# Kernel optimization log

Hardware: AMD Instinct MI355X
Metric: run time of the kernel (lower is better)

The kernel has to match this reference:

```python
import jax, jax.numpy as jnp
import numpy as np

HIDDEN = 512
HEADS = 8
HEAD_DIM = HIDDEN // HEADS
MAX_DIST = 10
B, N = 16, 512
EPS = 1e-5


def _layer_norm(x, g, b):
    mu = jnp.mean(x, axis=-1, keepdims=True)
    var = jnp.mean(jnp.square(x - mu), axis=-1, keepdims=True)
    return (x - mu) * jax.lax.rsqrt(var + EPS) * g + b


def setup_inputs() -> dict:
    key = jax.random.key(0)
    ks = jax.random.split(key, 16)
    s = 0.02
    inp = {
        "x": jax.random.normal(ks[0], (B, N, HIDDEN), jnp.float32),
        "distances": jax.random.randint(ks[1], (B, N, N), 0, MAX_DIST, jnp.int32),
        "edge_features": jax.random.normal(ks[2], (B, N, N), jnp.float32),
        "attn_mask": jax.random.randint(ks[3], (B, N), 0, 2).astype(bool),
        "Wq": jax.random.normal(ks[4], (HIDDEN, HIDDEN), jnp.float32) * s,
        "bq": jnp.zeros((HIDDEN,), jnp.float32),
        "Wk": jax.random.normal(ks[5], (HIDDEN, HIDDEN), jnp.float32) * s,
        "bk": jnp.zeros((HIDDEN,), jnp.float32),
        "Wv": jax.random.normal(ks[6], (HIDDEN, HIDDEN), jnp.float32) * s,
        "bv": jnp.zeros((HIDDEN,), jnp.float32),
        "Wo": jax.random.normal(ks[7], (HIDDEN, HIDDEN), jnp.float32) * s,
        "bo": jnp.zeros((HIDDEN,), jnp.float32),
        "spatial_emb": jax.random.normal(ks[8], (MAX_DIST, HEADS), jnp.float32) * s,
        "edge_w": jax.random.normal(ks[9], (HEADS,), jnp.float32) * s,
        "edge_b": jnp.zeros((HEADS,), jnp.float32),
        "ln1_g": jnp.ones((HIDDEN,), jnp.float32),
        "ln1_b": jnp.zeros((HIDDEN,), jnp.float32),
        "ln2_g": jnp.ones((HIDDEN,), jnp.float32),
        "ln2_b": jnp.zeros((HIDDEN,), jnp.float32),
        "W1": jax.random.normal(ks[10], (HIDDEN, 4 * HIDDEN), jnp.float32) * s,
        "b1": jnp.zeros((4 * HIDDEN,), jnp.float32),
        "W2": jax.random.normal(ks[11], (4 * HIDDEN, HIDDEN), jnp.float32) * s,
        "b2": jnp.zeros((HIDDEN,), jnp.float32),
    }
    return inp


def reference(x, distances, edge_features, attn_mask, Wq, bq, Wk, bk, Wv, bv,
              Wo, bo, spatial_emb, edge_w, edge_b, ln1_g, ln1_b, ln2_g, ln2_b,
              W1, b1, W2, b2):
    b, n, _ = x.shape
    q = (x @ Wq + bq).reshape(b, n, HEADS, HEAD_DIM)
    k = (x @ Wk + bk).reshape(b, n, HEADS, HEAD_DIM)
    v = (x @ Wv + bv).reshape(b, n, HEADS, HEAD_DIM)
    # [b, h, i, j] attention scores
    scores = jnp.einsum('bihd,bjhd->bhij', q, k) / np.sqrt(HEAD_DIM).astype(np.float32)
    spatial_bias = spatial_emb[distances]                       # [b, i, j, h]
    edge_bias = edge_features[..., None] * edge_w + edge_b      # [b, i, j, h]
    scores = scores + jnp.transpose(spatial_bias + edge_bias, (0, 3, 1, 2))
    scores = jnp.where(attn_mask[:, None, None, :], -jnp.inf, scores)
    attn = jax.nn.softmax(scores, axis=-1)
    out = jnp.einsum('bhij,bjhd->bihd', attn, v).reshape(b, n, HIDDEN)
    out = out @ Wo + bo
    h = _layer_norm(x + out, ln1_g, ln1_b)
    ffn = jax.nn.relu(h @ W1 + b1) @ W2 + b2
    return _layer_norm(h + ffn, ln2_g, ln2_b)
```

## Files before the change

### kernel.cpp

```cpp
#include <hip/hip_runtime.h>
#include <stdint.h>
#include <stddef.h>

#define SEQ   512
#define HID   512
#define NHEAD 8
#define HD    64
#define NBATCH 16
#define NTOK  8192
#define MAXD  10

typedef __attribute__((ext_vector_type(8))) short short8;
typedef __attribute__((ext_vector_type(4))) float f32x4;

typedef __attribute__((address_space(3))) void        as3_void;
typedef const __attribute__((address_space(1))) void  as1_cvoid;

#define MFMA16(a,b,c) __builtin_amdgcn_mfma_f32_16x16x32_bf16((a),(b),(c),0,0,0)

__device__ __forceinline__ float bf2f(uint16_t u){ return __uint_as_float(((uint32_t)u)<<16); }
__device__ __forceinline__ uint16_t f2bf(float f){
  uint32_t i = __float_as_uint(f);
  return (uint16_t)((i + 0x7fffu + ((i>>16)&1u)) >> 16);
}

enum { EPI_BF16=0, EPI_F32=3, EPI_RELU=4 };

__global__ __launch_bounds__(256) void f2bf_kernel(
    const float* __restrict__ in, uint16_t* __restrict__ out, int n4)
{
  int i = blockIdx.x*256 + threadIdx.x;
  if (i < n4){
    float4 v = *(const float4*)(in + (size_t)i*4);
    *(ushort4*)(out + (size_t)i*4) =
        make_ushort4(f2bf(v.x), f2bf(v.y), f2bf(v.z), f2bf(v.w));
  }
}

__global__ __launch_bounds__(256) void transpose_all(
    const float* __restrict__ Wq, const float* __restrict__ Wk,
    const float* __restrict__ Wv, const float* __restrict__ Wo,
    const float* __restrict__ W1, const float* __restrict__ W2,
    uint16_t* __restrict__ tq, uint16_t* __restrict__ tk,
    uint16_t* __restrict__ tv, uint16_t* __restrict__ to_,
    uint16_t* __restrict__ t1, uint16_t* __restrict__ t2)
{
  __shared__ uint16_t tile[32][33];
  int id = blockIdx.x;
  const float* in; uint16_t* out; int R, C, tx, ty;
  if (id < 1024) {
    int m = id >> 8, loc = id & 255;
    in  = (m==0)?Wq:(m==1)?Wk:(m==2)?Wv:Wo;
    out = (m==0)?tq:(m==1)?tk:(m==2)?tv:to_;
    R = 512; C = 512; ty = loc>>4; tx = loc&15;
  } else if (id < 2048) {
    int loc = id-1024; in=W1; out=t1; R=512; C=2048; ty=loc>>6; tx=loc&63;
  } else {
    int loc = id-2048; in=W2; out=t2; R=2048; C=512; ty=loc>>4; tx=loc&15;
  }
  int bx = tx*32, by = ty*32;
  int lx = threadIdx.x & 31, ly = threadIdx.x >> 5;
  #pragma unroll
  for (int i=ly; i<32; i+=8) tile[i][lx] = f2bf(in[(size_t)(by+i)*C + bx+lx]);
  __syncthreads();
  #pragma unroll
  for (int i=ly; i<32; i+=8) out[(size_t)(bx+i)*R + by+lx] = tile[lx][i];
}

__global__ __launch_bounds__(512) void pack_bias(
    const int*   __restrict__ dist,
    const float* __restrict__ edge,
    const int*   __restrict__ mask,
    uint32_t*    __restrict__ outp)
{
  __shared__ int   dl[16][260];
  __shared__ float el[16][260];
  __shared__ int   ml[512];
  const int b  = blockIdx.y;
  const int it = blockIdx.x;
  const int t  = threadIdx.x;
  ml[t] = mask[b*SEQ + t];

  #pragma unroll
  for (int jh=0; jh<2; ++jh){
    if (jh) __syncthreads();
    {
      const int r  = t >> 5;
      const int c0 = (t & 31) * 8;
      const size_t g = ((size_t)b*SEQ + it*16 + r)*SEQ + jh*256 + c0;
      *(int4*)&dl[r][c0]     = *(const int4*)&dist[g];
      *(int4*)&dl[r][c0+4]   = *(const int4*)&dist[g+4];
      *(float4*)&el[r][c0]   = *(const float4*)&edge[g];
      *(float4*)&el[r][c0+4] = *(const float4*)&edge[g+4];
    }
    __syncthreads();
    {
      const int i   = t & 15;
      const int j0p = (t >> 4) * 8;
      const int jt  = jh*4 + (j0p >> 6);
      const int jn  = (j0p >> 4) & 3;
      const int lg  = (j0p & 15) >> 2;
      uint32_t w[8];
      #pragma unroll
      for (int e=0; e<8; ++e){
        const int jl = j0p + e;
        const int jg = jh*256 + jl;
        const uint32_t d  = (uint32_t)dl[i][jl] & 0xFFu;
        const uint32_t mk = (ml[jg] ? 1u : 0u) << 8;
        w[e] = ((uint32_t)f2bf(el[i][jl]) << 16) | mk | d;
      }
      uint32_t* ob = outp + ((((size_t)b*32 + it)*8 + jt)*64)*16;
      const int lane0 = lg*16 + i, lane1 = (lg+1)*16 + i;
      *(uint4*)&ob[lane0*16 + jn*4] = make_uint4(w[0],w[1],w[2],w[3]);
      *(uint4*)&ob[lane1*16 + jn*4] = make_uint4(w[4],w[5],w[6],w[7]);
    }
  }
}

template<int BM, int BN>
__device__ __forceinline__ void gemm_tile_mainloop(
    const uint16_t* __restrict__ A, const uint16_t* __restrict__ Bt,
    int K, int m0, int n0, uint16_t* lA, uint16_t* lB,
    f32x4 acc[4][(BM==128)?4:((BN==128)?2:1)])
{
  constexpr int NJ  = (BM==128)?4:((BN==128)?2:1);
  constexpr int ARD = BM/32;
  constexpr int BRD = BN/32;
  const int t = threadIdx.x;
  const int w = t>>6, l = t&63;
  const int lg = l>>4, lc = l&15;
  const int wr = (BM==128)?(w>>1):0;
  const int wc = (BM==128)?(w&1):w;
  const int swz = lc & 7;
  const int kSteps = K>>6;
  for (int kt=0; kt<kSteps; ++kt){
    const int k0 = kt<<6;
    #pragma unroll
    for (int rd=0; rd<ARD; ++rd){
      const int e   = rd*2048 + t*8;
      const int row = e>>6;
      const int col = (((e>>3)&7) ^ (row&7))*8;
      const uint16_t* ga = A + (size_t)(m0+row)*K + (k0+col);
      char* la = (char*)lA + rd*4096 + w*1024;
      __builtin_amdgcn_global_load_lds((as1_cvoid*)ga, (as3_void*)la, 16, 0, 0);
    }
    #pragma unroll
    for (int rd=0; rd<BRD; ++rd){
      const int e   = rd*2048 + t*8;
      const int row = e>>6;
      const int col = (((e>>3)&7) ^ (row&7))*8;
      const uint16_t* gb = Bt + (size_t)(n0+row)*K + (k0+col);
      char* lb = (char*)lB + rd*4096 + w*1024;
      __builtin_amdgcn_global_load_lds((as1_cvoid*)gb, (as3_void*)lb, 16, 0, 0);
    }
    __syncthreads();
    #pragma unroll
    for (int kk=0; kk<2; ++kk){
      const int cc = (kk*4 + lg) ^ swz;
      short8 af[4], bfr[NJ];
      #pragma unroll
      for (int i=0;i<4;i++)
        af[i]  = *(const short8*)&lA[(wr*64 + i*16 + lc)*64 + cc*8];
      #pragma unroll
      for (int j=0;j<NJ;j++)
        bfr[j] = *(const short8*)&lB[(wc*16*NJ + j*16 + lc)*64 + cc*8];
      #pragma unroll
      for (int i=0;i<4;i++)
        #pragma unroll
        for (int j=0;j<NJ;j++)
          acc[i][j] = MFMA16(af[i], bfr[j], acc[i][j]);
    }
    __syncthreads();
  }
}

template<int EPI, int BM, int BN>
__global__ __launch_bounds__(256,2) void gemm_bt(
    const uint16_t* __restrict__ A, const uint16_t* __restrict__ Bt,
    const float* __restrict__ bias, void* __restrict__ outp,
    int M, int N, int K)
{
  constexpr int NJ = (BM==128)?4:((BN==128)?2:1);
  __shared__ uint16_t lA[BM*64];
  __shared__ uint16_t lB[BN*64];
  f32x4 acc[4][NJ];
  #pragma unroll
  for (int i=0;i<4;i++)
    #pragma unroll
    for (int j=0;j<NJ;j++){ f32x4 z = {0.f,0.f,0.f,0.f}; acc[i][j]=z; }
  const int m0 = blockIdx.x*BM, n0 = blockIdx.y*BN;
  gemm_tile_mainloop<BM,BN>(A, Bt, K, m0, n0, lA, lB, acc);

  const int t=threadIdx.x, w=t>>6, l=t&63, lg=l>>4, lc=l&15;
  const int wr=(BM==128)?(w>>1):0, wc=(BM==128)?(w&1):w;
  #pragma unroll
  for (int j=0;j<NJ;j++){
    const int col = n0 + wc*16*NJ + j*16 + lc;
    const float bs = bias[col];
    #pragma unroll
    for (int i=0;i<4;i++){
      const int rowb = m0 + wr*64 + i*16 + lg*4;
      #pragma unroll
      for (int r=0;r<4;r++){
        float v = acc[i][j][r] + bs;
        if constexpr (EPI==EPI_RELU)   v = fmaxf(v, 0.f);
        if constexpr (EPI==EPI_F32)
          ((float*)outp)[(size_t)(rowb+r)*N + col] = v;
        else
          ((uint16_t*)outp)[(size_t)(rowb+r)*N + col] = f2bf(v);
      }
    }
  }
}

__global__ __launch_bounds__(256,2) void qkv_gemm(
    const uint16_t* __restrict__ x,
    const uint16_t* __restrict__ wtq, const uint16_t* __restrict__ wtk,
    const uint16_t* __restrict__ wtv,
    const float* __restrict__ bq, const float* __restrict__ bk,
    const float* __restrict__ bv,
    uint16_t* __restrict__ qo, uint16_t* __restrict__ kp,
    uint16_t* __restrict__ vp)
{
  __shared__ uint16_t lA[128*64];
  __shared__ uint16_t lB[128*64];
  const int z = blockIdx.z;
  const uint16_t* Bt = (z==0)?wtq:(z==1)?wtk:wtv;
  const float*  bias = (z==0)?bq :(z==1)?bk :bv;
  f32x4 acc[4][4];
  #pragma unroll
  for (int i=0;i<4;i++)
    #pragma unroll
    for (int j=0;j<4;j++){ f32x4 zz = {0.f,0.f,0.f,0.f}; acc[i][j]=zz; }
  const int m0 = blockIdx.x*128, n0 = blockIdx.y*128;
  gemm_tile_mainloop<128,128>(x, Bt, HID, m0, n0, lA, lB, acc);

  const int t=threadIdx.x, w=t>>6, l=t&63, lg=l>>4, lc=l&15, wr=w>>1, wc=w&1;
  if (z==0){
    const float scale = 0.125f;
    #pragma unroll
    for (int j=0;j<4;j++){
      const int col = n0 + wc*64 + j*16 + lc;
      const float bs = bias[col];
      #pragma unroll
      for (int i=0;i<4;i++){
        const int rowb = m0 + wr*64 + i*16 + lg*4;
        #pragma unroll
        for (int r=0;r<4;r++)
          qo[(size_t)(rowb+r)*HID + col] = f2bf((acc[i][j][r] + bs)*scale);
      }
    }
  } else if (z==1){
    #pragma unroll
    for (int j=0;j<4;j++){
      const int col = n0 + wc*64 + j*16 + lc;
      const float bs = bias[col];
      const int h_ = col>>6, cm = col&63, kk = cm>>5, lgk = (cm>>3)&3, e = col&7;
      #pragma unroll
      for (int i=0;i<4;i++){
        const int rowb = m0 + wr*64 + i*16 + lg*4;
        #pragma unroll
        for (int r=0;r<4;r++){
          const int tok = rowb + r;
          const int b_ = tok>>9, tl = tok&511;
          const int jt = tl>>6, jn = (tl>>4)&3, lck = tl&15;
          kp[((((size_t)(b_*8+h_)*8 + jt)*4 + jn)*2 + kk)*512
             + (lgk*16 + lck)*8 + e] = f2bf(acc[i][j][r] + bs);
        }
      }
    }
  } else {
    #pragma unroll
    for (int j=0;j<4;j++){
      const int col = n0 + wc*64 + j*16 + lc;
      const float bs = bias[col];
      const int h_ = col>>6, dn = (col>>4)&3, lcv = col&15;
      #pragma unroll
      for (int i=0;i<4;i++){
        const int rowb = m0 + wr*64 + i*16 + lg*4;
        const int b_ = rowb>>9, tl = rowb&511;
        const int jt = tl>>6, kk = (tl>>5)&1, lgv = (tl>>3)&3, e0 = tl&7;
        *(ushort4*)&vp[((((size_t)(b_*8+h_)*8 + jt)*2 + kk)*4 + dn)*512
                       + (lgv*16 + lcv)*8 + e0] =
            make_ushort4(f2bf(acc[i][j][0]+bs), f2bf(acc[i][j][1]+bs),
                         f2bf(acc[i][j][2]+bs), f2bf(acc[i][j][3]+bs));
      }
    }
  }
}

__global__ __launch_bounds__(512,4) void attn_kernel(
    const uint16_t* __restrict__ q,
    const uint16_t* __restrict__ kp,
    const uint16_t* __restrict__ vp,
    const uint32_t* __restrict__ biasp,
    const float*    __restrict__ semb,
    const float*    __restrict__ ew,
    const float*    __restrict__ eb,
    uint16_t* __restrict__ out)
{
  __shared__ float sp_rep[NHEAD][32][11];
  __shared__ uint16_t plds[NHEAD][2][16*64];
  const int b  = blockIdx.y;
  const int it = blockIdx.x;
  const int i0 = it*16;
  const int t  = threadIdx.x;
  const int h  = t>>6, l = t&63, lg = l>>4, lc = l&15;
  for (int i = t; i < NHEAD*32*MAXD; i += 512){
    const int hh = i / (32*MAXD), rem = i % (32*MAXD);
    const int a = rem / MAXD, d = rem % MAXD;
    sp_rep[hh][a][d] = semb[d*NHEAD + hh];
  }
  __syncthreads();
  const float ewf = ew[h], ebf = eb[h];
  const float* spl = &sp_rep[h][l&31][0];
  char* pbase = (char*)&plds[h][0][0];
  const int swz = (lc&7)<<4;

  short8 qf[2];
  #pragma unroll
  for (int kk=0;kk<2;kk++)
    qf[kk] = *(const short8*)&q[(size_t)(b*SEQ + i0 + lc)*HID + h*HD + kk*32 + lg*8];

  const uint4* bp = (const uint4*)(biasp + (((size_t)b*32 + it)*8)*64*16);
  const uint16_t* kpb = kp + (size_t)(b*8+h)*8*4*2*512 + l*8;
  const uint16_t* vpb = vp + (size_t)(b*8+h)*8*2*4*512 + l*8;

  float mrun[2] = {-1e30f, -1e30f};
  float lrun[2] = {0.f, 0.f};
  f32x4 oacc[2][4];
  #pragma unroll
  for (int s=0;s<2;s++)
    #pragma unroll
    for (int dn=0;dn<4;dn++){ f32x4 z={0.f,0.f,0.f,0.f}; oacc[s][dn]=z; }

  #pragma unroll
  for (int p=0; p<4; ++p){
    #pragma unroll
    for (int s=0; s<2; ++s){
      const int jt = s*4 + p;
      uint32_t uw[16];
      {
        const uint4* bq_ = bp + (jt*64 + l)*4;
        *(uint4*)&uw[0]  = bq_[0];
        *(uint4*)&uw[4]  = bq_[1];
        *(uint4*)&uw[8]  = bq_[2];
        *(uint4*)&uw[12] = bq_[3];
      }
      f32x4 st[4];
      #pragma unroll
      for (int jn=0;jn<4;jn++){ f32x4 z={0.f,0.f,0.f,0.f}; st[jn]=z; }
      __builtin_amdgcn_s_setprio(1);
      #pragma unroll
      for (int jn=0;jn<4;jn++){
        #pragma unroll
        for (int kk=0;kk<2;kk++){
          short8 kf = *(const short8*)&kpb[(size_t)((jt*4 + jn)*2 + kk)*512];
          st[jn] = MFMA16(kf, qf[kk], st[jn]);
        }
      }
      __builtin_amdgcn_s_setprio(0);
      float tmax = -1e30f;
      #pragma unroll
      for (int jn=0;jn<4;jn++){
        #pragma unroll
        for (int r=0;r<4;r++){
          const uint32_t u = uw[jn*4+r];
          float sv = st[jn][r] + spl[u & 0xFFu]
                   + bf2f((uint16_t)(u >> 16))*ewf + ebf;
          if (u & 0x100u) sv = -1e30f;
          st[jn][r] = sv;
          tmax = fmaxf(tmax, sv);
        }
      }
      {
        float tm = fmaxf(tmax, __shfl_xor(tmax, 16, 64));
        tm = fmaxf(tm, __shfl_xor(tm, 32, 64));
        float mnew = fmaxf(mrun[s], tm);
        mnew = fmaxf(mnew, -1e20f);
        const float c = __expf(mrun[s] - mnew);
        mrun[s] = mnew;
        float lsum = 0.f;
        char* pb = pbase + s*(16*64*2) + lc*128;
        #pragma unroll
        for (int jn=0;jn<4;jn++){
          float p0 = __expf(st[jn][0]-mnew);
          float p1 = __expf(st[jn][1]-mnew);
          float p2 = __expf(st[jn][2]-mnew);
          float p3 = __expf(st[jn][3]-mnew);
          lsum += (p0+p1)+(p2+p3);
          *(ushort4*)(pb + (((jn*16 + lg*4)*2) ^ swz)) =
              make_ushort4(f2bf(p0), f2bf(p1), f2bf(p2), f2bf(p3));
        }
        lrun[s] = lrun[s]*c + lsum;
        #pragma unroll
        for (int r=0;r<4;r++){
          const float cr = __shfl(c, lg*4+r, 64);
          #pragma unroll
          for (int dn=0;dn<4;dn++) oacc[s][dn][r] *= cr;
        }
      }
    }
    #pragma unroll
    for (int s=0; s<2; ++s){
      const int jt = s*4 + p;
      char* pb = pbase + s*(16*64*2) + lc*128;
      __builtin_amdgcn_s_setprio(1);
      #pragma unroll
      for (int kk=0;kk<2;kk++){
        short8 pa = *(const short8*)(pb + (((kk*32 + lg*8)*2) ^ swz));
        #pragma unroll
        for (int dn=0;dn<4;dn++){
          short8 vb = *(const short8*)&vpb[(size_t)((jt*2 + kk)*4 + dn)*512];
          oacc[s][dn] = MFMA16(pa, vb, oacc[s][dn]);
        }
      }
      __builtin_amdgcn_s_setprio(0);
    }
  }
  {
    const float mm = fmaxf(mrun[0], mrun[1]);
    const float c0 = __expf(mrun[0]-mm), c1 = __expf(mrun[1]-mm);
    float ls = lrun[0]*c0 + lrun[1]*c1;
    ls += __shfl_xor(ls, 16, 64);
    ls += __shfl_xor(ls, 32, 64);
    const float inv = 1.f/ls;
    #pragma unroll
    for (int r=0;r<4;r++){
      const float cr0 = __shfl(c0, lg*4+r, 64);
      const float cr1 = __shfl(c1, lg*4+r, 64);
      const float ir  = __shfl(inv, lg*4+r, 64);
      const size_t orow = ((size_t)b*SEQ + i0 + lg*4 + r)*HID;
      #pragma unroll
      for (int dn=0;dn<4;dn++)
        out[orow + h*HD + dn*16 + lc] =
            f2bf((oacc[0][dn][r]*cr0 + oacc[1][dn][r]*cr1)*ir);
    }
  }
}

__global__ __launch_bounds__(256) void ln_kernel(
    const float* __restrict__ a, const float* __restrict__ bsrc,
    const float* __restrict__ g, const float* __restrict__ bb,
    float* __restrict__ of, uint16_t* __restrict__ ob)
{
  const int row = blockIdx.x*4 + (threadIdx.x>>6);
  const int l = threadIdx.x & 63;
  const float* ar = a    + (size_t)row*HID;
  const float* br = bsrc + (size_t)row*HID;
  float u[8];
  {
    float4 a0 = *(const float4*)(ar + l*4);
    float4 a1 = *(const float4*)(ar + 256 + l*4);
    float4 b0 = *(const float4*)(br + l*4);
    float4 b1 = *(const float4*)(br + 256 + l*4);
    u[0]=a0.x+b0.x; u[1]=a0.y+b0.y; u[2]=a0.z+b0.z; u[3]=a0.w+b0.w;
    u[4]=a1.x+b1.x; u[5]=a1.y+b1.y; u[6]=a1.z+b1.z; u[7]=a1.w+b1.w;
  }
  float s=0.f, ss=0.f;
  #pragma unroll
  for (int e=0;e<8;e++){ s += u[e]; ss += u[e]*u[e]; }
  #pragma unroll
  for (int off=32; off>=1; off>>=1){
    s  += __shfl_xor(s,  off, 64);
    ss += __shfl_xor(ss, off, 64);
  }
  const float mu  = s*(1.f/512.f);
  const float inv = rsqrtf(ss*(1.f/512.f) - mu*mu + 1e-5f);
  float y[8];
  #pragma unroll
  for (int e=0;e<4;e++){
    int c0 = l*4+e, c1 = 256+l*4+e;
    y[e]   = (u[e]  -mu)*inv*g[c0] + bb[c0];
    y[4+e] = (u[4+e]-mu)*inv*g[c1] + bb[c1];
  }
  if (of){
    float* orow = of + (size_t)row*HID;
    *(float4*)(orow + l*4)       = make_float4(y[0],y[1],y[2],y[3]);
    *(float4*)(orow + 256 + l*4) = make_float4(y[4],y[5],y[6],y[7]);
  }
  if (ob){
    uint16_t* brow = ob + (size_t)row*HID;
    *(ushort4*)(brow + l*4)       = make_ushort4(f2bf(y[0]),f2bf(y[1]),f2bf(y[2]),f2bf(y[3]));
    *(ushort4*)(brow + 256 + l*4) = make_ushort4(f2bf(y[4]),f2bf(y[5]),f2bf(y[6]),f2bf(y[7]));
  }
}

extern "C" void kernel_launch(void* const* d_in, const int* in_sizes, int n_in,
                              void* d_out, int out_size, void* d_ws, size_t ws_size,
                              hipStream_t stream)
{
  (void)in_sizes; (void)n_in; (void)out_size; (void)ws_size;
  const float* x    = (const float*)d_in[0];
  const int*   dist = (const int*)  d_in[1];
  const float* edge = (const float*)d_in[2];
  const int*   mask = (const int*)  d_in[3];
  const float* Wq = (const float*)d_in[4];
  const float* bq = (const float*)d_in[5];
  const float* Wk = (const float*)d_in[6];
  const float* bk = (const float*)d_in[7];
  const float* Wv = (const float*)d_in[8];
  const float* bv = (const float*)d_in[9];
  const float* Wo = (const float*)d_in[10];
  const float* bo = (const float*)d_in[11];
  const float* semb = (const float*)d_in[12];
  const float* ew   = (const float*)d_in[13];
  const float* eb   = (const float*)d_in[14];
  const float* ln1g = (const float*)d_in[15];
  const float* ln1b = (const float*)d_in[16];
  const float* ln2g = (const float*)d_in[17];
  const float* ln2b = (const float*)d_in[18];
  const float* W1 = (const float*)d_in[19];
  const float* b1 = (const float*)d_in[20];
  const float* W2 = (const float*)d_in[21];
  const float* b2 = (const float*)d_in[22];

  char* ws = (char*)d_ws;
  uint16_t* xb16  = (uint16_t*)ws;
  uint16_t* qbuf  = xb16  + (size_t)NTOK*HID;
  uint16_t* kpbuf = qbuf  + (size_t)NTOK*HID;
  uint16_t* vpbuf = kpbuf + (size_t)NTOK*HID;
  uint16_t* aobuf = vpbuf + (size_t)NTOK*HID;
  uint16_t* f1buf = qbuf;
  uint32_t* biasp = (uint32_t*)(ws + (size_t)5*NTOK*HID*2);
  float*    tbuf  = (float*)biasp;
  float*    t2buf = tbuf;
  float*    hbuf  = tbuf + (size_t)NTOK*HID;
  uint16_t* hb16  = (uint16_t*)(hbuf + (size_t)NTOK*HID);
  uint16_t* wt    = hb16 + (size_t)NTOK*HID;
  uint16_t* wtq = wt;
  uint16_t* wtk = wtq + 512*512;
  uint16_t* wtv = wtk + 512*512;
  uint16_t* wto = wtv + 512*512;
  uint16_t* wt1 = wto + 512*512;
  uint16_t* wt2 = wt1 + 512*2048;

  pack_bias<<<dim3(32,16), 512, 0, stream>>>(dist, edge, mask, biasp);

  transpose_all<<<3072, 256, 0, stream>>>(Wq,Wk,Wv,Wo,W1,W2, wtq,wtk,wtv,wto,wt1,wt2);

  f2bf_kernel<<<4096, 256, 0, stream>>>(x, xb16, NTOK*HID/4);

  qkv_gemm<<<dim3(64,4,3), 256, 0, stream>>>(xb16, wtq,wtk,wtv, bq,bk,bv,
                                             qbuf, kpbuf, vpbuf);

  attn_kernel<<<dim3(32,16), 512, 0, stream>>>(qbuf, kpbuf, vpbuf, biasp,
                                               semb, ew, eb, aobuf);

  gemm_bt<EPI_F32,64,64><<<dim3(128,8), 256, 0, stream>>>(aobuf, wto, bo, tbuf, NTOK, HID, HID);

  ln_kernel<<<2048, 256, 0, stream>>>(tbuf, x, ln1g, ln1b, hbuf, hb16);

  gemm_bt<EPI_RELU,128,128><<<dim3(64,16), 256, 0, stream>>>(hb16, wt1, b1, f1buf, NTOK, 2048, HID);

  gemm_bt<EPI_F32,64,64><<<dim3(128,8), 256, 0, stream>>>(f1buf, wt2, b2, t2buf, NTOK, HID, 2048);

  ln_kernel<<<2048, 256, 0, stream>>>(t2buf, hbuf, ln2g, ln2b, (float*)d_out, nullptr);
}
```

Baseline: 163.2 us.

## Double-buffer GEMM LDS tiles and streamline attention softmax with exp2 and lazy rescale

The GEMM mainloop now double-buffers its LDS tiles, issuing the global-to-LDS loads for the next K step before computing on the current one, which doubles shared memory per block. The attention kernel folds log2(e) into the Q scale and the bias tables and uses exp2. It merges the edge bias into the spatial table, packs bf16 pairs with v_cvt_pk_bf16, and skips the running-max rescale when the tile max stays within a threshold of the current max. The lazy rescale lets probabilities exceed 1 by up to 2^8, which risks a small change in precision, and the larger LDS footprint may reduce occupancy.

Measured after the change: 194.0 us. +18.8%, slower.

```diff
diff --git a/kernel.cpp b/kernel.cpp
--- a/kernel.cpp
+++ b/kernel.cpp
@@ -9,6 +9,7 @@
 #define NBATCH 16
 #define NTOK  8192
 #define MAXD  10
+#define LOG2E 1.4426950408889634f
 
 typedef __attribute__((ext_vector_type(8))) short short8;
 typedef __attribute__((ext_vector_type(4))) float f32x4;
@@ -22,6 +23,11 @@
 __device__ __forceinline__ uint16_t f2bf(float f){
   uint32_t i = __float_as_uint(f);
   return (uint16_t)((i + 0x7fffu + ((i>>16)&1u)) >> 16);
+}
+__device__ __forceinline__ uint32_t cvt_pk_bf16(float lo, float hi){
+  uint32_t r;
+  asm("v_cvt_pk_bf16_f32 %0, %1, %2" : "=v"(r) : "v"(lo), "v"(hi));
+  return r;
 }
 
 enum { EPI_BF16=0, EPI_F32=3, EPI_RELU=4 };
@@ -133,7 +139,8 @@
   const int wc = (BM==128)?(w&1):w;
   const int swz = lc & 7;
   const int kSteps = K>>6;
-  for (int kt=0; kt<kSteps; ++kt){
+
+  auto stage = [&](int kt, int buf){
     const int k0 = kt<<6;
     #pragma unroll
     for (int rd=0; rd<ARD; ++rd){
@@ -141,7 +148,7 @@
       const int row = e>>6;
       const int col = (((e>>3)&7) ^ (row&7))*8;
       const uint16_t* ga = A + (size_t)(m0+row)*K + (k0+col);
-      char* la = (char*)lA + rd*4096 + w*1024;
+      char* la = (char*)(lA + buf*(BM*64)) + rd*4096 + w*1024;
       __builtin_amdgcn_global_load_lds((as1_cvoid*)ga, (as3_void*)la, 16, 0, 0);
     }
     #pragma unroll
@@ -150,20 +157,28 @@
       const int row = e>>6;
       const int col = (((e>>3)&7) ^ (row&7))*8;
       const uint16_t* gb = Bt + (size_t)(n0+row)*K + (k0+col);
-      char* lb = (char*)lB + rd*4096 + w*1024;
+      char* lb = (char*)(lB + buf*(BN*64)) + rd*4096 + w*1024;
       __builtin_amdgcn_global_load_lds((as1_cvoid*)gb, (as3_void*)lb, 16, 0, 0);
     }
-    __syncthreads();
+  };
+
+  stage(0, 0);
+  __syncthreads();
+  int cur = 0;
+  for (int kt=0; kt<kSteps; ++kt){
+    if (kt+1 < kSteps) stage(kt+1, cur^1);
+    const uint16_t* rA = lA + cur*(BM*64);
+    const uint16_t* rB = lB + cur*(BN*64);
     #pragma unroll
     for (int kk=0; kk<2; ++kk){
       const int cc = (kk*4 + lg) ^ swz;
       short8 af[4], bfr[NJ];
       #pragma unroll
       for (int i=0;i<4;i++)
-        af[i]  = *(const short8*)&lA[(wr*64 + i*16 + lc)*64 + cc*8];
+        af[i]  = *(const short8*)&rA[(wr*64 + i*16 + lc)*64 + cc*8];
       #pragma unroll
       for (int j=0;j<NJ;j++)
-        bfr[j] = *(const short8*)&lB[(wc*16*NJ + j*16 + lc)*64 + cc*8];
+        bfr[j] = *(const short8*)&rB[(wc*16*NJ + j*16 + lc)*64 + cc*8];
       #pragma unroll
       for (int i=0;i<4;i++)
         #pragma unroll
@@ -171,6 +186,7 @@
           acc[i][j] = MFMA16(af[i], bfr[j], acc[i][j]);
     }
     __syncthreads();
+    cur ^= 1;
   }
 }
 
@@ -181,8 +197,8 @@
     int M, int N, int K)
 {
   constexpr int NJ = (BM==128)?4:((BN==128)?2:1);
-  __shared__ uint16_t lA[BM*64];
-  __shared__ uint16_t lB[BN*64];
+  __shared__ uint16_t lA[2*BM*64];
+  __shared__ uint16_t lB[2*BN*64];
   f32x4 acc[4][NJ];
   #pragma unroll
   for (int i=0;i<4;i++)
@@ -222,8 +238,8 @@
     uint16_t* __restrict__ qo, uint16_t* __restrict__ kp,
     uint16_t* __restrict__ vp)
 {
-  __shared__ uint16_t lA[128*64];
-  __shared__ uint16_t lB[128*64];
+  __shared__ uint16_t lA[2*128*64];
+  __shared__ uint16_t lB[2*128*64];
   const int z = blockIdx.z;
   const uint16_t* Bt = (z==0)?wtq:(z==1)?wtk:wtv;
   const float*  bias = (z==0)?bq :(z==1)?bk :bv;
@@ -237,7 +253,7 @@
 
   const int t=threadIdx.x, w=t>>6, l=t&63, lg=l>>4, lc=l&15, wr=w>>1, wc=w&1;
   if (z==0){
-    const float scale = 0.125f;
+    const float scale = 0.125f * LOG2E;
     #pragma unroll
     for (int j=0;j<4;j++){
       const int col = n0 + wc*64 + j*16 + lc;
@@ -309,10 +325,10 @@
   for (int i = t; i < NHEAD*32*MAXD; i += 512){
     const int hh = i / (32*MAXD), rem = i % (32*MAXD);
     const int a = rem / MAXD, d = rem % MAXD;
-    sp_rep[hh][a][d] = semb[d*NHEAD + hh];
+    sp_rep[hh][a][d] = (semb[d*NHEAD + hh] + eb[hh]) * LOG2E;
   }
   __syncthreads();
-  const float ewf = ew[h], ebf = eb[h];
+  const float ewf = ew[h] * LOG2E;
   const float* spl = &sp_rep[h][l&31][0];
   char* pbase = (char*)&plds[h][0][0];
   const int swz = (lc&7)<<4;
@@ -367,7 +383,7 @@
         for (int r=0;r<4;r++){
           const uint32_t u = uw[jn*4+r];
           float sv = st[jn][r] + spl[u & 0xFFu]
-                   + bf2f((uint16_t)(u >> 16))*ewf + ebf;
+                   + bf2f((uint16_t)(u >> 16))*ewf;
           if (u & 0x100u) sv = -1e30f;
           st[jn][r] = sv;
           tmax = fmaxf(tmax, sv);
@@ -376,28 +392,34 @@
       {
         float tm = fmaxf(tmax, __shfl_xor(tmax, 16, 64));
         tm = fmaxf(tm, __shfl_xor(tm, 32, 64));
-        float mnew = fmaxf(mrun[s], tm);
-        mnew = fmaxf(mnew, -1e20f);
-        const float c = __expf(mrun[s] - mnew);
-        mrun[s] = mnew;
+        const bool need = !__all((tm <= mrun[s] + 8.0f) && (mrun[s] > -1e25f));
+        float c = 1.f;
+        if (need){
+          float mnew = fmaxf(fmaxf(mrun[s], tm), -1e20f);
+          c = __builtin_amdgcn_exp2f(mrun[s] - mnew);
+          mrun[s] = mnew;
+        }
+        const float mcur = mrun[s];
         float lsum = 0.f;
         char* pb = pbase + s*(16*64*2) + lc*128;
         #pragma unroll
         for (int jn=0;jn<4;jn++){
-          float p0 = __expf(st[jn][0]-mnew);
-          float p1 = __expf(st[jn][1]-mnew);
-          float p2 = __expf(st[jn][2]-mnew);
-          float p3 = __expf(st[jn][3]-mnew);
+          float p0 = __builtin_amdgcn_exp2f(st[jn][0]-mcur);
+          float p1 = __builtin_amdgcn_exp2f(st[jn][1]-mcur);
+          float p2 = __builtin_amdgcn_exp2f(st[jn][2]-mcur);
+          float p3 = __builtin_amdgcn_exp2f(st[jn][3]-mcur);
           lsum += (p0+p1)+(p2+p3);
-          *(ushort4*)(pb + (((jn*16 + lg*4)*2) ^ swz)) =
-              make_ushort4(f2bf(p0), f2bf(p1), f2bf(p2), f2bf(p3));
+          *(uint2*)(pb + (((jn*16 + lg*4)*2) ^ swz)) =
+              make_uint2(cvt_pk_bf16(p0,p1), cvt_pk_bf16(p2,p3));
         }
         lrun[s] = lrun[s]*c + lsum;
-        #pragma unroll
-        for (int r=0;r<4;r++){
-          const float cr = __shfl(c, lg*4+r, 64);
+        if (need){
           #pragma unroll
-          for (int dn=0;dn<4;dn++) oacc[s][dn][r] *= cr;
+          for (int r=0;r<4;r++){
+            const float cr = __shfl(c, lg*4+r, 64);
+            #pragma unroll
+            for (int dn=0;dn<4;dn++) oacc[s][dn][r] *= cr;
+          }
         }
       }
     }
@@ -420,7 +442,8 @@
   }
   {
     const float mm = fmaxf(mrun[0], mrun[1]);
-    const float c0 = __expf(mrun[0]-mm), c1 = __expf(mrun[1]-mm);
+    const float c0 = __builtin_amdgcn_exp2f(mrun[0]-mm);
+    const float c1 = __builtin_amdgcn_exp2f(mrun[1]-mm);
     float ls = lrun[0]*c0 + lrun[1]*c1;
     ls += __shfl_xor(ls, 16, 64);
     ls += __shfl_xor(ls, 32, 64);
```
